# Performance work log

Hardware: AMD Instinct MI355X
Metric: run time of the kernel (lower is better)

Reference implementation:

```python
import jax, jax.numpy as jnp
import numpy as np

B, DIM, N = 8, 512, 1024
EMB, CDIM, M = 128, 512, 256
HEADS, DHEAD = 8, 64
DFF = 4 * DIM  # GEGLU inner dim


def _group_norm(x, g, b, groups=32, eps=1e-6):
    # x: [B, C, L]
    Bx, C, L = x.shape
    xr = x.reshape(Bx, groups, (C // groups) * L)
    mu = xr.mean(-1, keepdims=True)
    var = xr.var(-1, keepdims=True)
    xn = ((xr - mu) * jax.lax.rsqrt(var + eps)).reshape(Bx, C, L)
    return xn * g[None, :, None] + b[None, :, None]


def _layer_norm(x, g, b, eps=1e-5):
    mu = x.mean(-1, keepdims=True)
    var = x.var(-1, keepdims=True)
    return (x - mu) * jax.lax.rsqrt(var + eps) * g + b


def _attention(x, ctx, wq, wk, wv, wo, bo, heads):
    # x: [B, Nq, Dq], ctx: [B, Nk, Dk]
    Bx, Nq, _ = x.shape
    q = x @ wq.T
    k = ctx @ wk.T
    v = ctx @ wv.T
    d = q.shape[-1] // heads
    sp = lambda t: t.reshape(Bx, -1, heads, d).transpose(0, 2, 1, 3)  # b h n d
    q, k, v = sp(q), sp(k), sp(v)
    sim = jnp.einsum('bhid,bhjd->bhij', q, k) * (d ** -0.5)
    o = jnp.einsum('bhij,bhjd->bhid', jax.nn.softmax(sim, axis=-1), v)
    o = o.transpose(0, 2, 1, 3).reshape(Bx, Nq, heads * d)
    return o @ wo.T + bo


def setup_inputs() -> dict:
    key = jax.random.key(0)
    ks = jax.random.split(key, 16)
    rn = lambda k, sh: jax.random.normal(k, sh, dtype=jnp.float32) * 0.02
    inner = HEADS * DHEAD
    z = lambda n: jnp.zeros((n,), jnp.float32)
    o = lambda n: jnp.ones((n,), jnp.float32)
    return {
        'x': jax.random.normal(ks[0], (B, DIM, N), dtype=jnp.float32),
        'emb': jax.random.normal(ks[1], (B, EMB), dtype=jnp.float32),
        'context': jax.random.normal(ks[2], (B, CDIM, M), dtype=jnp.float32),
        'w_emb': rn(ks[3], (2 * DIM, EMB)), 'b_emb': z(2 * DIM),
        'gn_g': o(DIM), 'gn_b': z(DIM),
        'conv_w': rn(ks[4], (DIM, DIM)), 'conv_b': z(DIM),
        'a1_wq': rn(ks[5], (inner, DIM)), 'a1_wk': rn(ks[6], (inner, DIM)),
        'a1_wv': rn(ks[7], (inner, DIM)), 'a1_wo': rn(ks[8], (DIM, inner)), 'a1_bo': z(DIM),
        'a2_wq': rn(ks[9], (inner, DIM)), 'a2_wk': rn(ks[10], (inner, CDIM)),
        'a2_wv': rn(ks[11], (inner, CDIM)), 'a2_wo': rn(ks[12], (DIM, inner)), 'a2_bo': z(DIM),
        'ln1_g': o(DIM), 'ln1_b': z(DIM),
        'ln2_g': o(DIM), 'ln2_b': z(DIM),
        'ln3_g': o(DIM), 'ln3_b': z(DIM),
        'ff_w1': rn(ks[13], (2 * DFF, DIM)), 'ff_b1': z(2 * DFF),
        'ff_w2': rn(ks[14], (DIM, DFF)), 'ff_b2': z(DIM),
    }


def reference(x, emb, context, w_emb, b_emb, gn_g, gn_b, conv_w, conv_b,
              a1_wq, a1_wk, a1_wv, a1_wo, a1_bo,
              a2_wq, a2_wk, a2_wv, a2_wo, a2_bo,
              ln1_g, ln1_b, ln2_g, ln2_b, ln3_g, ln3_b,
              ff_w1, ff_b1, ff_w2, ff_b2):
    # scale-shift modulated GroupNorm + SiLU + 1x1 Conv1d residual branch
    emb_out = (jax.nn.silu(emb) @ w_emb.T + b_emb)[:, :, None]  # [B, 2*dim, 1]
    scale, shift = jnp.split(emb_out, 2, axis=1)
    h = _group_norm(x, gn_g, gn_b) * (1.0 + scale) + shift
    h = jnp.einsum('oc,bcn->bon', conv_w, jax.nn.silu(h)) + conv_b[None, :, None]
    x = x + h
    # to token-major layout
    xt = x.transpose(0, 2, 1)          # [B, N, dim]
    ctx = context.transpose(0, 2, 1)   # [B, M, context_dim]
    # self attention
    y = _layer_norm(xt, ln1_g, ln1_b)
    xt = _attention(y, y, a1_wq, a1_wk, a1_wv, a1_wo, a1_bo, HEADS) + xt
    # cross attention
    xt = _attention(_layer_norm(xt, ln2_g, ln2_b), ctx,
                    a2_wq, a2_wk, a2_wv, a2_wo, a2_bo, HEADS) + xt
    # GEGLU feed-forward
    u = _layer_norm(xt, ln3_g, ln3_b) @ ff_w1.T + ff_b1
    a, g = jnp.split(u, 2, axis=-1)
    xt = (a * jax.nn.gelu(g, approximate=False)) @ ff_w2.T + ff_b2 + xt
    return xt.transpose(0, 2, 1)  # back to [B, dim, N]
```

## Files before the change

### kernel.cpp

```cpp
#include <hip/hip_runtime.h>
#include <math.h>

#define NB 8
#define CDIM 512
#define NT 1024
#define MT 256
#define DFFI 2048

typedef short bf16x8 __attribute__((ext_vector_type(8)));
typedef float f32x4 __attribute__((ext_vector_type(4)));

__device__ __forceinline__ float sigmoidf_(float v){ return 1.0f/(1.0f+__expf(-v)); }

__device__ __forceinline__ short f2bf(float f){
    union { float f; unsigned u; } v; v.f = f;
    unsigned r = v.u + 0x7FFFu + ((v.u >> 16) & 1u);
    return (short)(r >> 16);
}

__device__ __forceinline__ unsigned pk2bf(float lo, float hi){
    union { float f; unsigned u; } a, b; a.f = lo; b.f = hi;
    return (a.u >> 16) | (b.u & 0xFFFF0000u);
}

#define GLDS(gp, lp) __builtin_amdgcn_global_load_lds( \
    (const __attribute__((address_space(1))) void*)(gp), \
    (__attribute__((address_space(3))) void*)(lp), 16, 0, 0)

__global__ void cvt_all(const float* __restrict__ a1wq, const float* __restrict__ a1wk,
                        const float* __restrict__ a1wv, const float* __restrict__ a1wo,
                        const float* __restrict__ a2wq, const float* __restrict__ a2wk,
                        const float* __restrict__ a2wv, const float* __restrict__ a2wo,
                        const float* __restrict__ ffw1, const float* __restrict__ ffw2,
                        const float* __restrict__ convw, short* __restrict__ WB){
    int e = (blockIdx.x*256 + threadIdx.x)*8;
    if (e >= 5505024) return;
    const float* src; int off;
    if (e < 2097152){
        const float* tbl[8] = {a1wq,a1wk,a1wv,a1wo,a2wq,a2wk,a2wv,a2wo};
        src = tbl[e >> 18]; off = e & 262143;
    } else if (e < 4194304){ src = ffw1; off = e - 2097152; }
    else if (e < 5242880){ src = ffw2; off = e - 4194304; }
    else { src = convw; off = e - 5242880; }
    float4 x0 = ((const float4*)(src+off))[0], x1 = ((const float4*)(src+off))[1];
    bf16x8 v;
    v[0]=f2bf(x0.x); v[1]=f2bf(x0.y); v[2]=f2bf(x0.z); v[3]=f2bf(x0.w);
    v[4]=f2bf(x1.x); v[5]=f2bf(x1.y); v[6]=f2bf(x1.z); v[7]=f2bf(x1.w);
    *(bf16x8*)(WB + e) = v;
}


__global__ void emb_gemm(const float* __restrict__ emb, const float* __restrict__ w,
                         const float* __restrict__ bias, float* __restrict__ out){
    int idx = blockIdx.x*256 + threadIdx.x;
    int b = idx >> 10, o = idx & 1023;
    const float* e = emb + b*128;
    const float* wr = w + (size_t)o*128;
    float acc = 0.f;
    for (int i=0;i<128;i++){ float ev=e[i]; acc += (ev*sigmoidf_(ev))*wr[i]; }
    out[idx] = acc + bias[o];
}

__global__ void gn_stats(const float* __restrict__ x, float* __restrict__ stats){
    int bg = blockIdx.x;
    const float* base = x + (size_t)bg*16*NT;
    float s=0.f, sq=0.f;
    for (int i=threadIdx.x; i<16*NT; i+=256){ float v = base[i]; s+=v; sq+=v*v; }
    __shared__ float rs[256], rq[256];
    rs[threadIdx.x]=s; rq[threadIdx.x]=sq; __syncthreads();
    for (int st=128; st>0; st>>=1){
        if (threadIdx.x<st){ rs[threadIdx.x]+=rs[threadIdx.x+st]; rq[threadIdx.x]+=rq[threadIdx.x+st]; }
        __syncthreads();
    }
    if (threadIdx.x==0){
        float mu = rs[0]/(16.f*NT);
        float var = rq[0]/(16.f*NT) - mu*mu;
        stats[2*bg] = mu; stats[2*bg+1] = rsqrtf(var + 1e-6f);
    }
}

__global__ void mod_act(const float* __restrict__ x, const float* __restrict__ stats,
                        const float* __restrict__ gg, const float* __restrict__ gb,
                        const float* __restrict__ ss, short* __restrict__ act_t){
    __shared__ float tile[32][33];
    int n0 = blockIdx.x*32, c0 = blockIdx.y*32, b = blockIdx.z;
    int tx = threadIdx.x, ty = threadIdx.y;
    #pragma unroll
    for (int k=0;k<4;k++){
        int c = c0 + ty + k*8;
        tile[ty+k*8][tx] = x[((size_t)(b*CDIM+c))*NT + n0 + tx];
    }
    __syncthreads();
    #pragma unroll
    for (int k=0;k<4;k++){
        int c = c0 + tx, n = n0 + ty + k*8;
        float raw = tile[tx][ty+k*8];
        int gi = b*32 + (c>>4);
        float v = (raw - stats[2*gi]) * stats[2*gi+1] * gg[c] + gb[c];
        v = v * (1.f + ss[b*1024 + c]) + ss[b*1024 + 512 + c];
        act_t[((size_t)(b*NT+n))*CDIM + c] = f2bf(v * sigmoidf_(v));
    }
}

__global__ void ln_rows(const float* __restrict__ in, const float* __restrict__ g,
                        const float* __restrict__ bta, short* __restrict__ out){
    int row = blockIdx.x*4 + (threadIdx.x>>6);
    int lane = threadIdx.x & 63;
    const float* base = in + (size_t)row*CDIM + lane*8;
    float4 a = ((const float4*)base)[0], b4 = ((const float4*)base)[1];
    float vals[8] = {a.x,a.y,a.z,a.w,b4.x,b4.y,b4.z,b4.w};
    float s = 0.f, q = 0.f;
    #pragma unroll
    for (int i=0;i<8;i++){ s += vals[i]; q += vals[i]*vals[i]; }
    #pragma unroll
    for (int off=32; off>0; off>>=1){ s += __shfl_xor(s, off); q += __shfl_xor(q, off); }
    float mu = s*(1.f/512.f);
    float rstd = rsqrtf(q*(1.f/512.f) - mu*mu + 1e-5f);
    const float* gp = g + lane*8;
    const float* bp = bta + lane*8;
    float4 g0=((const float4*)gp)[0], g1=((const float4*)gp)[1];
    float4 e0=((const float4*)bp)[0], e1=((const float4*)bp)[1];
    float gs[8] = {g0.x,g0.y,g0.z,g0.w,g1.x,g1.y,g1.z,g1.w};
    float es[8] = {e0.x,e0.y,e0.z,e0.w,e1.x,e1.y,e1.z,e1.w};
    bf16x8 o8;
    #pragma unroll
    for (int i=0;i<8;i++) o8[i] = f2bf((vals[i]-mu)*rstd*gs[i] + es[i]);
    *(bf16x8*)(out + (size_t)row*CDIM + lane*8) = o8;
}

__global__ void transpose_ctx(const float* __restrict__ in, short* __restrict__ out){
    __shared__ float tile[32][33];
    int m0 = blockIdx.x*32, c0 = blockIdx.y*32, b = blockIdx.z;
    int tx=threadIdx.x, ty=threadIdx.y;
    #pragma unroll
    for (int k=0;k<4;k++){
        int c = c0+ty+k*8;
        tile[ty+k*8][tx] = in[((size_t)(b*512+c))*MT + m0+tx];
    }
    __syncthreads();
    #pragma unroll
    for (int k=0;k<4;k++){
        int m = m0+ty+k*8, c = c0+tx;
        out[((size_t)(b*MT+m))*512 + c] = f2bf(tile[tx][ty+k*8]);
    }
}

__global__ void transpose_out(const float* __restrict__ in, float* __restrict__ out){
    __shared__ float tile[32][33];
    int n0 = blockIdx.x*32, c0 = blockIdx.y*32, b=blockIdx.z;
    int tx=threadIdx.x, ty=threadIdx.y;
    #pragma unroll
    for (int k=0;k<4;k++){
        int n = n0+ty+k*8;
        tile[ty+k*8][tx] = in[((size_t)(b*NT+n))*512 + c0+tx];
    }
    __syncthreads();
    #pragma unroll
    for (int k=0;k<4;k++){
        int c = c0+ty+k*8, n = n0+tx;
        out[((size_t)(b*512+c))*NT + n] = tile[tx][ty+k*8];
    }
}

__global__ __launch_bounds__(256,2) void gemm_bb(
        const short* __restrict__ A, const short* __restrict__ W,
        const float* __restrict__ bias, const float* __restrict__ res,
        float* __restrict__ outf, short* __restrict__ outb,
        int K, int O, int ostr, int resmode){
    __shared__ short As[128*64];
    __shared__ short Bs[64*64];
    int r0 = blockIdx.x*128, o0 = blockIdx.y*64;
    int tid = threadIdx.x, w = tid>>6, lane = tid&63;
    int quad = lane>>4, lw = lane&15;
    int g_row = lane>>3, g_s = lane&7;
    int sseg = g_s ^ g_row;
    int wr = (w&1)*64, wc = (w>>1)*32;
    f32x4 acc[4][2] = {};
    for (int k0 = 0; k0 < K; k0 += 64){
        #pragma unroll
        for (int j=0;j<4;j++){
            int row = w*32 + j*8 + g_row;
            GLDS(A + (size_t)(r0+row)*K + k0 + sseg*8, As + (w*32+j*8)*64);
        }
        #pragma unroll
        for (int j=0;j<2;j++){
            int row = w*16 + j*8 + g_row;
            GLDS(W + (size_t)(o0+row)*K + k0 + sseg*8, Bs + (w*16+j*8)*64);
        }
        __syncthreads();
        bf16x8 af[4][2], bf[2][2];
        #pragma unroll
        for (int ks=0; ks<2; ks++){
            #pragma unroll
            for (int i=0;i<4;i++){
                int row = wr + i*16 + lw;
                af[i][ks] = *(const bf16x8*)&As[row*64 + (((ks*4+quad) ^ (lw&7)))*8];
            }
            #pragma unroll
            for (int j=0;j<2;j++){
                int col = wc + j*16 + lw;
                bf[j][ks] = *(const bf16x8*)&Bs[col*64 + (((ks*4+quad) ^ (lw&7)))*8];
            }
        }
        #pragma unroll
        for (int ks=0; ks<2; ks++)
            #pragma unroll
            for (int i=0;i<4;i++)
                #pragma unroll
                for (int j=0;j<2;j++)
                    acc[i][j] = __builtin_amdgcn_mfma_f32_16x16x32_bf16(af[i][ks], bf[j][ks], acc[i][j], 0, 0, 0);
        __syncthreads();
    }
    #pragma unroll
    for (int i=0;i<4;i++){
        #pragma unroll
        for (int j=0;j<2;j++){
            #pragma unroll
            for (int reg=0; reg<4; reg++){
                int row = r0 + wr + i*16 + quad*4 + reg;
                int col = o0 + wc + j*16 + lw;
                float v = acc[i][j][reg];
                if (bias) v += bias[col];
                if (resmode==1) v += res[(size_t)row*O + col];
                else if (resmode==2){
                    int b = row >> 10, n = row & 1023;
                    v += res[((size_t)(b*CDIM+col))*NT + n];
                }
                if (outf) outf[(size_t)row*ostr + col] = v;
                else      outb[(size_t)row*ostr + col] = f2bf(v);
            }
        }
    }
}

__global__ __launch_bounds__(256) void gemm64(
        const short* __restrict__ A, const short* __restrict__ W,
        const float* __restrict__ bias, const float* __restrict__ res,
        float* __restrict__ outf, short* __restrict__ outb,
        int K, int O, int ostr, int resmode){
    __shared__ short As[64*64];
    __shared__ short Bs[64*64];
    int r0 = blockIdx.x*64, o0 = blockIdx.y*64;
    int tid = threadIdx.x, w = tid>>6, lane = tid&63;
    int quad = lane>>4, lw = lane&15;
    int lrow = lane>>3, lg = (lane&7) ^ (lane>>3);
    int wr = (w&1)*32, wc = (w>>1)*32;
    f32x4 acc[2][2] = {};
    for (int k0 = 0; k0 < K; k0 += 64){
        #pragma unroll
        for (int t=0;t<2;t++){
            int row = w*16 + t*8 + lrow;
            GLDS(A + (size_t)(r0+row)*K + k0 + lg*8, As + (w*16+t*8)*64);
            GLDS(W + (size_t)(o0+row)*K + k0 + lg*8, Bs + (w*16+t*8)*64);
        }
        __syncthreads();
        bf16x8 af[2][2], bf[2][2];
        #pragma unroll
        for (int ks=0; ks<2; ks++){
            #pragma unroll
            for (int i=0;i<2;i++){
                int row = wr + i*16 + lw;
                af[i][ks] = *(const bf16x8*)&As[row*64 + (((ks*4+quad) ^ (lw&7)))*8];
                int col = wc + i*16 + lw;
                bf[i][ks] = *(const bf16x8*)&Bs[col*64 + (((ks*4+quad) ^ (lw&7)))*8];
            }
        }
        #pragma unroll
        for (int ks=0; ks<2; ks++)
            #pragma unroll
            for (int i=0;i<2;i++)
                #pragma unroll
                for (int j=0;j<2;j++)
                    acc[i][j] = __builtin_amdgcn_mfma_f32_16x16x32_bf16(af[i][ks], bf[j][ks], acc[i][j], 0, 0, 0);
        __syncthreads();
    }
    #pragma unroll
    for (int i=0;i<2;i++){
        #pragma unroll
        for (int j=0;j<2;j++){
            #pragma unroll
            for (int reg=0; reg<4; reg++){
                int row = r0 + wr + i*16 + quad*4 + reg;
                int col = o0 + wc + j*16 + lw;
                float v = acc[i][j][reg];
                if (bias) v += bias[col];
                if (resmode==1) v += res[(size_t)row*O + col];
                else if (resmode==2){
                    int b = row >> 10, n = row & 1023;
                    v += res[((size_t)(b*CDIM+col))*NT + n];
                }
                if (outf) outf[(size_t)row*ostr + col] = v;
                else      outb[(size_t)row*ostr + col] = f2bf(v);
            }
        }
    }
}

__global__ __launch_bounds__(256,2) void ff1_geglu_bb(
        const short* __restrict__ A, const short* __restrict__ W,
        const float* __restrict__ b1, short* __restrict__ out){
    __shared__ short As[128*64];
    __shared__ short Ba[64*64];
    __shared__ short Bg[64*64];
    int r0 = blockIdx.x*128, j0 = blockIdx.y*64;
    int tid = threadIdx.x, w = tid>>6, lane = tid&63;
    int quad = lane>>4, lw = lane&15;
    int g_row = lane>>3, g_s = lane&7;
    int sseg = g_s ^ g_row;
    int wr = (w&1)*64, wc = (w>>1)*32;
    f32x4 acca[4][2] = {}, accg[4][2] = {};
    for (int k0 = 0; k0 < 512; k0 += 64){
        #pragma unroll
        for (int j=0;j<4;j++){
            int row = w*32 + j*8 + g_row;
            GLDS(A + (size_t)(r0+row)*512 + k0 + sseg*8, As + (w*32+j*8)*64);
        }
        #pragma unroll
        for (int j=0;j<2;j++){
            int row = w*16 + j*8 + g_row;
            GLDS(W + (size_t)(j0+row)*512 + k0 + sseg*8, Ba + (w*16+j*8)*64);
            GLDS(W + (size_t)(2048+j0+row)*512 + k0 + sseg*8, Bg + (w*16+j*8)*64);
        }
        __syncthreads();
        bf16x8 af[4][2], ba[2][2], bg[2][2];
        #pragma unroll
        for (int ks=0; ks<2; ks++){
            #pragma unroll
            for (int i=0;i<4;i++){
                int row = wr + i*16 + lw;
                af[i][ks] = *(const bf16x8*)&As[row*64 + (((ks*4+quad) ^ (lw&7)))*8];
            }
            #pragma unroll
            for (int j=0;j<2;j++){
                int col = wc + j*16 + lw;
                ba[j][ks] = *(const bf16x8*)&Ba[col*64 + (((ks*4+quad) ^ (lw&7)))*8];
                bg[j][ks] = *(const bf16x8*)&Bg[col*64 + (((ks*4+quad) ^ (lw&7)))*8];
            }
        }
        #pragma unroll
        for (int ks=0; ks<2; ks++)
            #pragma unroll
            for (int i=0;i<4;i++)
                #pragma unroll
                for (int j=0;j<2;j++){
                    acca[i][j] = __builtin_amdgcn_mfma_f32_16x16x32_bf16(af[i][ks], ba[j][ks], acca[i][j], 0, 0, 0);
                    accg[i][j] = __builtin_amdgcn_mfma_f32_16x16x32_bf16(af[i][ks], bg[j][ks], accg[i][j], 0, 0, 0);
                }
        __syncthreads();
    }
    #pragma unroll
    for (int i=0;i<4;i++){
        #pragma unroll
        for (int j=0;j<2;j++){
            #pragma unroll
            for (int reg=0; reg<4; reg++){
                int row = r0 + wr + i*16 + quad*4 + reg;
                int col = j0 + wc + j*16 + lw;
                float a = acca[i][j][reg] + b1[col];
                float g = accg[i][j][reg] + b1[2048+col];
                float gl = 0.5f*g*(1.0f + erff(g*0.70710678118654752f));
                out[(size_t)row*DFFI + col] = f2bf(a*gl);
            }
        }
    }
}

__global__ __launch_bounds__(256) void attn_fa(
        const short* __restrict__ q, const short* __restrict__ k,
        const short* __restrict__ vt, short* __restrict__ o,
        int Nq, int Nk, int qstr, int kstr, int vtstr, float sc_log2e){
    __shared__ short Ks[64*64];
    __shared__ short Vs[64*64];
    __shared__ short Qs[64*64];
    int bh = blockIdx.x & 63;
    int qt = blockIdx.x >> 6;
    int b = bh >> 3, h = bh & 7;
    int tid = threadIdx.x, w = tid>>6, lane = tid&63;
    int quad = lane>>4, lw = lane&15;
    int lrow = lane>>3, lg = (lane&7) ^ (lane>>3);
    int q0 = qt*64;

    #pragma unroll
    for (int t=0;t<2;t++){
        int row = w*16 + t*8 + lrow;
        GLDS(q + (size_t)(b*Nq + q0 + row)*qstr + h*64 + lg*8, Qs + (w*16+t*8)*64);
    }
    __syncthreads();
    bf16x8 qf[2];
    {
        int r = w*16 + lw;
        qf[0] = *(const bf16x8*)&Qs[r*64 + (( quad    ^ (r&7))*8)];
        qf[1] = *(const bf16x8*)&Qs[r*64 + (((quad+4) ^ (r&7))*8)];
    }

    f32x4 oacc[4] = {};
    f32x4 accl = {};
    bf16x8 ones;
    #pragma unroll
    for (int i=0;i<8;i++) ones[i] = (short)0x3F80;

    int x7 = lw&7;
    int nkt = Nk >> 6;
    for (int kt = 0; kt < nkt; kt++){
        __syncthreads();
        #pragma unroll
        for (int t=0;t<2;t++){
            int row = w*16 + t*8 + lrow;
            GLDS(k  + (size_t)(b*Nk + kt*64 + row)*kstr + h*64 + lg*8, Ks + (w*16+t*8)*64);
            GLDS(vt + (size_t)(h*64 + row)*vtstr + b*Nk + kt*64 + lg*8, Vs + (w*16+t*8)*64);
        }
        __syncthreads();

        f32x4 s[4];
        #pragma unroll
        for (int ct=0;ct<4;ct++){
            int r = ct*16 + lw;
            bf16x8 kf0 = *(const bf16x8*)&Ks[r*64 + (( quad    ^ (r&7))*8)];
            bf16x8 kf1 = *(const bf16x8*)&Ks[r*64 + (((quad+4) ^ (r&7))*8)];
            f32x4 z = {};
            z = __builtin_amdgcn_mfma_f32_16x16x32_bf16(kf0, qf[0], z, 0,0,0);
            s[ct] = __builtin_amdgcn_mfma_f32_16x16x32_bf16(kf1, qf[1], z, 0,0,0);
        }
        float pe[4][4];
        #pragma unroll
        for (int ct=0;ct<4;ct++)
            #pragma unroll
            for (int r=0;r<4;r++) pe[ct][r] = exp2f(s[ct][r]*sc_log2e);
        union { bf16x8 v; unsigned u[4]; } pa[2];
        #pragma unroll
        for (int pr=0;pr<2;pr++){
            pa[pr].u[0] = pk2bf(pe[pr*2  ][0], pe[pr*2  ][1]);
            pa[pr].u[1] = pk2bf(pe[pr*2  ][2], pe[pr*2  ][3]);
            pa[pr].u[2] = pk2bf(pe[pr*2+1][0], pe[pr*2+1][1]);
            pa[pr].u[3] = pk2bf(pe[pr*2+1][2], pe[pr*2+1][3]);
        }
        accl = __builtin_amdgcn_mfma_f32_16x16x32_bf16(pa[0].v, ones, accl, 0,0,0);
        accl = __builtin_amdgcn_mfma_f32_16x16x32_bf16(pa[1].v, ones, accl, 0,0,0);
        #pragma unroll
        for (int dt=0; dt<4; dt++){
            int rb = (dt*16 + lw)*64;
            #pragma unroll
            for (int pr=0;pr<2;pr++){
                int gl  = pr*4 + (quad>>1);
                int off = (quad&1)*4;
                union { bf16x8 v; unsigned long long d[2]; } vb;
                vb.d[0] = *(const unsigned long long*)&Vs[rb + (( gl    ^ x7)<<3) + off];
                vb.d[1] = *(const unsigned long long*)&Vs[rb + (((gl+2) ^ x7)<<3) + off];
                oacc[dt] = __builtin_amdgcn_mfma_f32_16x16x32_bf16(pa[pr].v, vb.v, oacc[dt], 0,0,0);
            }
        }
    }
    float inv[4];
    #pragma unroll
    for (int r=0;r<4;r++) inv[r] = 1.0f/accl[r];
    #pragma unroll
    for (int dt=0; dt<4; dt++){
        #pragma unroll
        for (int r=0;r<4;r++){
            int qi = q0 + w*16 + quad*4 + r;
            o[(size_t)(b*Nq + qi)*512 + h*64 + dt*16 + lw] = f2bf(oacc[dt][r]*inv[r]);
        }
    }
}

extern "C" void kernel_launch(void* const* d_in, const int* in_sizes, int n_in,
                              void* d_out, int out_size, void* d_ws, size_t ws_size,
                              hipStream_t stream) {
    const float* x      = (const float*)d_in[0];
    const float* emb    = (const float*)d_in[1];
    const float* context= (const float*)d_in[2];
    const float* w_emb  = (const float*)d_in[3];
    const float* b_emb  = (const float*)d_in[4];
    const float* gn_g   = (const float*)d_in[5];
    const float* gn_b   = (const float*)d_in[6];
    const float* conv_w = (const float*)d_in[7];
    const float* conv_b = (const float*)d_in[8];
    const float* a1_wq  = (const float*)d_in[9];
    const float* a1_wk  = (const float*)d_in[10];
    const float* a1_wv  = (const float*)d_in[11];
    const float* a1_wo  = (const float*)d_in[12];
    const float* a1_bo  = (const float*)d_in[13];
    const float* a2_wq  = (const float*)d_in[14];
    const float* a2_wk  = (const float*)d_in[15];
    const float* a2_wv  = (const float*)d_in[16];
    const float* a2_wo  = (const float*)d_in[17];
    const float* a2_bo  = (const float*)d_in[18];
    const float* ln1_g  = (const float*)d_in[19];
    const float* ln1_b  = (const float*)d_in[20];
    const float* ln2_g  = (const float*)d_in[21];
    const float* ln2_b  = (const float*)d_in[22];
    const float* ln3_g  = (const float*)d_in[23];
    const float* ln3_b  = (const float*)d_in[24];
    const float* ff_w1  = (const float*)d_in[25];
    const float* ff_b1  = (const float*)d_in[26];
    const float* ff_w2  = (const float*)d_in[27];
    const float* ff_b2  = (const float*)d_in[28];
    float* out = (float*)d_out;

    char* base = (char*)d_ws;
    float* SS    = (float*)base;
    float* STATS = SS + 8192;
    float* F0    = (float*)(base + 65536);
    float* F1    = F0 + 4194304;
    short* WB    = (short*)(F1 + 4194304);
    short* qkW   = WB;
    short* vW    = WB + 524288;
    short* wo1W  = WB + 786432;
    short* a2qW  = WB + 1048576;
    short* a2kW  = WB + 1310720;
    short* a2vW  = WB + 1572864;
    short* wo2W  = WB + 1835008;
    short* ffw1W = WB + 2097152;
    short* ffw2W = WB + 4194304;
    short* convW = WB + 5242880;
    short* CTXb  = WB + 5505024;
    short* L0    = CTXb + 1048576;
    short* BIG   = L0 + 4194304;
    short* Q0    = BIG;
    short* VT1   = BIG + 8388608;
    short* AO    = BIG + 12582912;
    short* A2Q   = BIG;
    short* K2    = BIG + 4194304;
    short* VT2   = BIG + 5242880;
    short* ACT2  = BIG;

    dim3 tb(32,8);
    const float SCL2E = 0.125f * 1.4426950408889634f;

    cvt_all<<<2688,256,0,stream>>>(a1_wq,a1_wk,a1_wv,a1_wo,a2_wq,a2_wk,a2_wv,a2_wo,
                                   ff_w1,ff_w2,conv_w, WB);

    emb_gemm<<<32,256,0,stream>>>(emb, w_emb, b_emb, SS);
    gn_stats<<<256,256,0,stream>>>(x, STATS);
    mod_act<<<dim3(32,16,8), tb, 0, stream>>>(x, STATS, gn_g, gn_b, SS, L0);
    transpose_ctx<<<dim3(8,16,8), tb, 0, stream>>>(context, CTXb);
    gemm64<<<dim3(128,8),256,0,stream>>>(L0, convW, conv_b, x, F0, nullptr, 512, 512, 512, 2);

    ln_rows<<<2048,256,0,stream>>>(F0, ln1_g, ln1_b, L0);
    gemm_bb<<<dim3(64,16),256,0,stream>>>(L0, qkW, nullptr, nullptr, nullptr, Q0, 512, 1024, 1024, 0);
    gemm64<<<dim3(8,128),256,0,stream>>>(vW, L0, nullptr, nullptr, nullptr, VT1, 512, 8192, 8192, 0);
    attn_fa<<<1024,256,0,stream>>>(Q0, Q0+512, VT1, AO, 1024, 1024, 1024, 1024, 8192, SCL2E);
    gemm64<<<dim3(128,8),256,0,stream>>>(AO, wo1W, a1_bo, F0, F1, nullptr, 512, 512, 512, 1);

    ln_rows<<<2048,256,0,stream>>>(F1, ln2_g, ln2_b, L0);
    gemm64<<<dim3(128,8),256,0,stream>>>(L0, a2qW, nullptr, nullptr, nullptr, A2Q, 512, 512, 512, 0);
    gemm64<<<dim3(32,8),256,0,stream>>>(CTXb, a2kW, nullptr, nullptr, nullptr, K2, 512, 512, 512, 0);
    gemm64<<<dim3(8,32),256,0,stream>>>(a2vW, CTXb, nullptr, nullptr, nullptr, VT2, 512, 2048, 2048, 0);
    attn_fa<<<1024,256,0,stream>>>(A2Q, K2, VT2, AO, 1024, 256, 512, 512, 2048, SCL2E);
    gemm64<<<dim3(128,8),256,0,stream>>>(AO, wo2W, a2_bo, F1, F0, nullptr, 512, 512, 512, 1);

    ln_rows<<<2048,256,0,stream>>>(F0, ln3_g, ln3_b, L0);
    ff1_geglu_bb<<<dim3(64,32),256,0,stream>>>(L0, ffw1W, ff_b1, ACT2);
    gemm64<<<dim3(128,8),256,0,stream>>>(ACT2, ffw2W, ff_b2, F0, F1, nullptr, 2048, 512, 512, 1);
    transpose_out<<<dim3(32,16,8), tb, 0, stream>>>(F1, out);
}
```

Measured before the change: 427.2 us.

## Split FF2 GEMM along K and shrink GEGLU tile to raise occupancy

```diff
diff --git a/kernel.cpp b/kernel.cpp
--- a/kernel.cpp
+++ b/kernel.cpp
@@ -145,14 +145,16 @@
     }
 }
 
-__global__ void transpose_out(const float* __restrict__ in, float* __restrict__ out){
+__global__ void transpose_out(const float* __restrict__ in1, const float* __restrict__ in2,
+                              float* __restrict__ out){
     __shared__ float tile[32][33];
     int n0 = blockIdx.x*32, c0 = blockIdx.y*32, b=blockIdx.z;
     int tx=threadIdx.x, ty=threadIdx.y;
     #pragma unroll
     for (int k=0;k<4;k++){
         int n = n0+ty+k*8;
-        tile[ty+k*8][tx] = in[((size_t)(b*NT+n))*512 + c0+tx];
+        size_t idx = ((size_t)(b*NT+n))*512 + c0+tx;
+        tile[ty+k*8][tx] = in1[idx] + in2[idx];
     }
     __syncthreads();
     #pragma unroll
@@ -237,7 +239,7 @@
         const short* __restrict__ A, const short* __restrict__ W,
         const float* __restrict__ bias, const float* __restrict__ res,
         float* __restrict__ outf, short* __restrict__ outb,
-        int K, int O, int ostr, int resmode){
+        int K, int astr, int wstr, int O, int ostr, int resmode){
     __shared__ short As[64*64];
     __shared__ short Bs[64*64];
     int r0 = blockIdx.x*64, o0 = blockIdx.y*64;
@@ -250,8 +252,8 @@
         #pragma unroll
         for (int t=0;t<2;t++){
             int row = w*16 + t*8 + lrow;
-            GLDS(A + (size_t)(r0+row)*K + k0 + lg*8, As + (w*16+t*8)*64);
-            GLDS(W + (size_t)(o0+row)*K + k0 + lg*8, Bs + (w*16+t*8)*64);
+            GLDS(A + (size_t)(r0+row)*astr + k0 + lg*8, As + (w*16+t*8)*64);
+            GLDS(W + (size_t)(o0+row)*wstr + k0 + lg*8, Bs + (w*16+t*8)*64);
         }
         __syncthreads();
         bf16x8 af[2][2], bf[2][2];
@@ -296,51 +298,43 @@
     }
 }
 
-__global__ __launch_bounds__(256,2) void ff1_geglu_bb(
+__global__ __launch_bounds__(256) void ff1_geglu64(
         const short* __restrict__ A, const short* __restrict__ W,
         const float* __restrict__ b1, short* __restrict__ out){
-    __shared__ short As[128*64];
+    __shared__ short As[64*64];
     __shared__ short Ba[64*64];
     __shared__ short Bg[64*64];
-    int r0 = blockIdx.x*128, j0 = blockIdx.y*64;
+    int r0 = blockIdx.x*64, j0 = blockIdx.y*64;
     int tid = threadIdx.x, w = tid>>6, lane = tid&63;
     int quad = lane>>4, lw = lane&15;
-    int g_row = lane>>3, g_s = lane&7;
-    int sseg = g_s ^ g_row;
-    int wr = (w&1)*64, wc = (w>>1)*32;
-    f32x4 acca[4][2] = {}, accg[4][2] = {};
+    int lrow = lane>>3, lg = (lane&7) ^ (lane>>3);
+    int wr = (w&1)*32, wc = (w>>1)*32;
+    f32x4 acca[2][2] = {}, accg[2][2] = {};
     for (int k0 = 0; k0 < 512; k0 += 64){
         #pragma unroll
-        for (int j=0;j<4;j++){
-            int row = w*32 + j*8 + g_row;
-            GLDS(A + (size_t)(r0+row)*512 + k0 + sseg*8, As + (w*32+j*8)*64);
-        }
-        #pragma unroll
-        for (int j=0;j<2;j++){
-            int row = w*16 + j*8 + g_row;
-            GLDS(W + (size_t)(j0+row)*512 + k0 + sseg*8, Ba + (w*16+j*8)*64);
-            GLDS(W + (size_t)(2048+j0+row)*512 + k0 + sseg*8, Bg + (w*16+j*8)*64);
-        }
-        __syncthreads();
-        bf16x8 af[4][2], ba[2][2], bg[2][2];
+        for (int t=0;t<2;t++){
+            int row = w*16 + t*8 + lrow;
+            GLDS(A + (size_t)(r0+row)*512 + k0 + lg*8, As + (w*16+t*8)*64);
+            GLDS(W + (size_t)(j0+row)*512 + k0 + lg*8, Ba + (w*16+t*8)*64);
+            GLDS(W + (size_t)(2048+j0+row)*512 + k0 + lg*8, Bg + (w*16+t*8)*64);
+        }
+        __syncthreads();
+        bf16x8 af[2][2], ba[2][2], bg[2][2];
         #pragma unroll
         for (int ks=0; ks<2; ks++){
             #pragma unroll
-            for (int i=0;i<4;i++){
+            for (int i=0;i<2;i++){
                 int row = wr + i*16 + lw;
                 af[i][ks] = *(const bf16x8*)&As[row*64 + (((ks*4+quad) ^ (lw&7)))*8];
-            }
-            #pragma unroll
-            for (int j=0;j<2;j++){
-                int col = wc + j*16 + lw;
-                ba[j][ks] = *(const bf16x8*)&Ba[col*64 + (((ks*4+quad) ^ (lw&7)))*8];
-                bg[j][ks] = *(const bf16x8*)&Bg[col*64 + (((ks*4+quad) ^ (lw&7)))*8];
+                int col = wc + i*16 + lw;
+                ba[i][ks] = *(const bf16x8*)&Ba[col*64 + (((ks*4+quad) ^ (lw&7)))*8];
+                bg[i][ks] = *(const bf16x8*)&Bg[col*64 + (((ks*4+quad) ^ (lw&7)))*8];
             }
         }
         #pragma unroll
         for (int ks=0; ks<2; ks++)
             #pragma unroll
-            for (int i=0;i<4;i++)
+            for (int i=0;i<2;i++)
                 #pragma unroll
                 for (int j=0;j<2;j++){
                     acca[i][j] = __builtin_amdgcn_mfma_f32_16x16x32_bf16(af[i][ks], ba[j][ks], acca[i][j], 0, 0, 0);
@@ -349,7 +343,7 @@
         __syncthreads();
     }
     #pragma unroll
-    for (int i=0;i<4;i++){
+    for (int i=0;i<2;i++){
         #pragma unroll
         for (int j=0;j<2;j++){
             #pragma unroll
@@ -502,7 +496,8 @@
     float* STATS = SS + 8192;
     float* F0    = (float*)(base + 65536);
     float* F1    = F0 + 4194304;
-    short* WB    = (short*)(F1 + 4194304);
+    float* F2    = F1 + 4194304;
+    short* WB    = (short*)(F2 + 4194304);
     short* qkW   = WB;
     short* vW    = WB + 524288;
     short* wo1W  = WB + 786432;
@@ -534,23 +529,24 @@
     gn_stats<<<256,256,0,stream>>>(x, STATS);
     mod_act<<<dim3(32,16,8), tb, 0, stream>>>(x, STATS, gn_g, gn_b, SS, L0);
     transpose_ctx<<<dim3(8,16,8), tb, 0, stream>>>(context, CTXb);
-    gemm64<<<dim3(128,8),256,0,stream>>>(L0, convW, conv_b, x, F0, nullptr, 512, 512, 512, 2);
+    gemm64<<<dim3(128,8),256,0,stream>>>(L0, convW, conv_b, x, F0, nullptr, 512,512,512, 512,512, 2);
 
     ln_rows<<<2048,256,0,stream>>>(F0, ln1_g, ln1_b, L0);
     gemm_bb<<<dim3(64,16),256,0,stream>>>(L0, qkW, nullptr, nullptr, nullptr, Q0, 512, 1024, 1024, 0);
-    gemm64<<<dim3(8,128),256,0,stream>>>(vW, L0, nullptr, nullptr, nullptr, VT1, 512, 8192, 8192, 0);
+    gemm64<<<dim3(8,128),256,0,stream>>>(vW, L0, nullptr, nullptr, nullptr, VT1, 512,512,512, 8192,8192, 0);
     attn_fa<<<1024,256,0,stream>>>(Q0, Q0+512, VT1, AO, 1024, 1024, 1024, 1024, 8192, SCL2E);
-    gemm64<<<dim3(128,8),256,0,stream>>>(AO, wo1W, a1_bo, F0, F1, nullptr, 512, 512, 512, 1);
+    gemm64<<<dim3(128,8),256,0,stream>>>(AO, wo1W, a1_bo, F0, F1, nullptr, 512,512,512, 512,512, 1);
 
     ln_rows<<<2048,256,0,stream>>>(F1, ln2_g, ln2_b, L0);
-    gemm64<<<dim3(128,8),256,0,stream>>>(L0, a2qW, nullptr, nullptr, nullptr, A2Q, 512, 512, 512, 0);
-    gemm64<<<dim3(32,8),256,0,stream>>>(CTXb, a2kW, nullptr, nullptr, nullptr, K2, 512, 512, 512, 0);
-    gemm64<<<dim3(8,32),256,0,stream>>>(a2vW, CTXb, nullptr, nullptr, nullptr, VT2, 512, 2048, 2048, 0);
+    gemm64<<<dim3(128,8),256,0,stream>>>(L0, a2qW, nullptr, nullptr, nullptr, A2Q, 512,512,512, 512,512, 0);
+    gemm64<<<dim3(32,8),256,0,stream>>>(CTXb, a2kW, nullptr, nullptr, nullptr, K2, 512,512,512, 512,512, 0);
+    gemm64<<<dim3(8,32),256,0,stream>>>(a2vW, CTXb, nullptr, nullptr, nullptr, VT2, 512,512,512, 2048,2048, 0);
     attn_fa<<<1024,256,0,stream>>>(A2Q, K2, VT2, AO, 1024, 256, 512, 512, 2048, SCL2E);
-    gemm64<<<dim3(128,8),256,0,stream>>>(AO, wo2W, a2_bo, F1, F0, nullptr, 512, 512, 512, 1);
+    gemm64<<<dim3(128,8),256,0,stream>>>(AO, wo2W, a2_bo, F1, F0, nullptr, 512,512,512, 512,512, 1);
 
     ln_rows<<<2048,256,0,stream>>>(F0, ln3_g, ln3_b, L0);
-    ff1_geglu_bb<<<dim3(64,32),256,0,stream>>>(L0, ffw1W, ff_b1, ACT2);
-    gemm64<<<dim3(128,8),256,0,stream>>>(ACT2, ffw2W, ff_b2, F0, F1, nullptr, 2048, 512, 512, 1);
-    transpose_out<<<dim3(32,16,8), tb, 0, stream>>>(F1, out);
-}
+    ff1_geglu64<<<dim3(128,32),256,0,stream>>>(L0, ffw1W, ff_b1, ACT2);
+    gemm64<<<dim3(128,8),256,0,stream>>>(ACT2,      ffw2W,      ff_b2,  F0,      F1, nullptr, 1024,2048,2048, 512,512, 1);
+    gemm64<<<dim3(128,8),256,0,stream>>>(ACT2+1024, ffw2W+1024, nullptr,nullptr, F2, nullptr, 1024,2048,2048, 512,512, 0);
+    transpose_out<<<dim3(32,16,8), tb, 0, stream>>>(F1, F2, out);
+}
```

Result: slower. 444.6 us (+4.1%).
